# Performance work log

Measured on AMD Instinct MI355X. Metric: run time of the kernel, lower is better.

## Reference

```python
import jax, jax.numpy as jnp
import numpy as np

IMG = 1024.0            # image H = W
PRE_NMS, POST_NMS = 2000, 1000
NMS_THR, MIN_SZ = 0.7, 16.0
B = 16                  # batch of images


def _make_anchors():
    # Standard FPN anchor tiling: strides {4..64}, one scale per level, 3 ratios.
    strides = [4, 8, 16, 32, 64]
    scales = [32.0, 64.0, 128.0, 256.0, 512.0]
    ratios = [0.5, 1.0, 2.0]
    out = []
    for s, sc in zip(strides, scales):
        n = int(IMG) // s
        c = (np.arange(n, dtype=np.float32) + 0.5) * s
        xs, ys = np.meshgrid(c, c, indexing="xy")
        ctr = np.stack([xs.ravel(), ys.ravel()], -1)              # (n*n, 2) cx,cy
        wh = np.array([[sc * np.sqrt(1.0 / r), sc * np.sqrt(r)] for r in ratios],
                      dtype=np.float32)                           # (3, 2)
        b = np.concatenate([ctr[:, None, :] - wh[None] / 2,
                            ctr[:, None, :] + wh[None] / 2], -1)  # (n*n, 3, 4)
        out.append(b.reshape(-1, 4))
    return np.concatenate(out, 0).astype(np.float32)              # (261888, 4)


def setup_inputs() -> dict:
    key = jax.random.key(0)
    k1, k2 = jax.random.split(key)
    anchors = jnp.asarray(_make_anchors())
    A = anchors.shape[0]
    deltas = jax.random.normal(k1, (B, A, 4), dtype=jnp.float32) * 0.1
    scores = jax.random.uniform(k2, (B, A), dtype=jnp.float32)    # post-sigmoid objectness
    return {"anchors": anchors, "deltas": deltas, "scores": scores}


def _decode(anchors, deltas):
    # decode_boxes: deltas (tx,ty,tw,th) applied to anchors; dw/dh clamped at 4.0
    aw = anchors[:, 2] - anchors[:, 0]
    ah = anchors[:, 3] - anchors[:, 1]
    ax = anchors[:, 0] + 0.5 * aw
    ay = anchors[:, 1] + 0.5 * ah
    dx, dy = deltas[..., 0], deltas[..., 1]
    dw = jnp.minimum(deltas[..., 2], 4.0)
    dh = jnp.minimum(deltas[..., 3], 4.0)
    px = dx * aw + ax
    py = dy * ah + ay
    pw = jnp.exp(dw) * aw
    ph = jnp.exp(dh) * ah
    return jnp.stack([px - 0.5 * pw, py - 0.5 * ph,
                      px + 0.5 * pw, py + 0.5 * ph], -1)


def _box_iou(a, b):
    area_a = (a[:, 2] - a[:, 0]) * (a[:, 3] - a[:, 1])
    area_b = (b[:, 2] - b[:, 0]) * (b[:, 3] - b[:, 1])
    lt = jnp.maximum(a[:, None, :2], b[None, :, :2])
    rb = jnp.minimum(a[:, None, 2:], b[None, :, 2:])
    wh = jnp.clip(rb - lt, 0.0)
    inter = wh[..., 0] * wh[..., 1]
    return inter / (area_a[:, None] + area_b[None, :] - inter + 1e-6)


def _filter_one(props, s):
    # RegionProposalNetwork._filter: clip -> size filter -> topk(pre_nms) -> NMS -> post_nms
    x1 = jnp.clip(props[:, 0], 0.0, IMG)
    y1 = jnp.clip(props[:, 1], 0.0, IMG)
    x2 = jnp.clip(props[:, 2], 0.0, IMG)
    y2 = jnp.clip(props[:, 3], 0.0, IMG)
    valid = (x2 - x1 >= MIN_SZ) & (y2 - y1 >= MIN_SZ)
    ms = jnp.where(valid, s, -jnp.inf)                 # mask instead of boolean gather (jit)
    vals, idx = jax.lax.top_k(ms, PRE_NMS)            # sorted desc, as in scores.topk
    b = jnp.stack([x1, y1, x2, y2], -1)[idx]          # (PRE_NMS, 4)
    iou = _box_iou(b, b)                              # (PRE_NMS, PRE_NMS)
    later = jnp.arange(PRE_NMS)

    def body(i, keep):
        # suppress later boxes overlapping a still-kept box i (greedy NMS)
        sup = (iou[i] > NMS_THR) & keep[i] & (later > i)
        return keep & ~sup

    keep = jax.lax.fori_loop(0, PRE_NMS, body, jnp.ones(PRE_NMS, dtype=bool))
    fs = jnp.where(keep, vals, -jnp.inf)
    fv, fi = jax.lax.top_k(fs, POST_NMS)              # kept boxes, desc score order
    good = jnp.isfinite(fv)                           # padding mask for suppressed slots
    boxes = jnp.where(good[:, None], b[fi], 0.0)
    sc = jnp.where(good, fv, 0.0)
    return jnp.concatenate([boxes, sc[:, None]], -1)  # (POST_NMS, 5) = (x1,y1,x2,y2,score)


def reference(anchors, deltas, scores):
    props = _decode(anchors, deltas)                  # (B, A, 4)
    return jax.vmap(_filter_one)(props, scores)       # (B, POST_NMS, 5)
```

## Files before the change

kernel.cpp:

```cpp
#include <hip/hip_runtime.h>
#include <stdint.h>
#include <math.h>


#define IMGF 1024.0f
#define PRE_NMS 2000
#define POST_NMS 1000
#define NMS_THR 0.7f
#define MIN_SZ 16.0f
#define CAP 4096
#define SEL 2048
#define NW (SEL / 64)
#define CNT_STRIDE 32
#define KEY_NEGINF 0x007FFFFFu
#define MAXCHUNK 12
#define IOU_T 0x1.6666668p-1

__device__ __forceinline__ uint32_t f2key(float f) {
  uint32_t u = __float_as_uint(f);
  return (u & 0x80000000u) ? ~u : (u | 0x80000000u);
}
__device__ __forceinline__ float key2f(uint32_t k) {
  uint32_t u = (k & 0x80000000u) ? (k & 0x7FFFFFFFu) : ~k;
  return __uint_as_float(u);
}

__device__ __forceinline__ unsigned long long readlane_u64(unsigned long long v,
                                                           int lane) {
  unsigned int lo = __builtin_amdgcn_readlane((unsigned int)v, lane);
  unsigned int hi = __builtin_amdgcn_readlane((unsigned int)(v >> 32), lane);
  return ((unsigned long long)hi << 32) | lo;
}

__device__ __forceinline__ float4 decode_clip(float4 anc, float4 dlt) {
  float aw = anc.z - anc.x;
  float ah = anc.w - anc.y;
  float ax = anc.x + 0.5f * aw;
  float ay = anc.y + 0.5f * ah;
  float dw = fminf(dlt.z, 4.0f);
  float dh = fminf(dlt.w, 4.0f);
  float px = dlt.x * aw + ax;
  float py = dlt.y * ah + ay;
  float pw = expf(dw) * aw;
  float ph = expf(dh) * ah;
  float x1 = px - 0.5f * pw, y1 = py - 0.5f * ph;
  float x2 = px + 0.5f * pw, y2 = py + 0.5f * ph;
  x1 = fminf(fmaxf(x1, 0.0f), IMGF);
  y1 = fminf(fmaxf(y1, 0.0f), IMGF);
  x2 = fminf(fmaxf(x2, 0.0f), IMGF);
  y2 = fminf(fmaxf(y2, 0.0f), IMGF);
  return make_float4(x1, y1, x2, y2);
}

__global__ void k_decode(const float4* __restrict__ anchors,
                         const float4* __restrict__ deltas,
                         const float* __restrict__ scores,
                         uint32_t* __restrict__ keys,
                         uint32_t* __restrict__ chist,
                         int A, int chunks) {
  int b = blockIdx.y;
  int t = threadIdx.x;
  int lane = t & 63;
  __shared__ uint32_t shist[256];
  shist[t] = 0;
  __syncthreads();
  int base_a = blockIdx.x * (chunks * 256);
  for (int c = 0; c < chunks; c++) {
    int a = base_a + c * 256 + t;
    bool inb = a < A;
    int ac = inb ? a : (A - 1);
    size_t i = (size_t)b * A + ac;
    float4 box = decode_clip(anchors[ac], deltas[i]);
    bool valid = (box.z - box.x >= MIN_SZ) && (box.w - box.y >= MIN_SZ);
    float ms = valid ? scores[i] : -INFINITY;
    uint32_t k = f2key(ms);
    if (inb) keys[i] = k;
    uint32_t bucket = k >> 24;
    bool fin = inb && (k != KEY_NEGINF);
    unsigned long long match = __ballot(fin);
#pragma unroll
    for (int bit = 0; bit < 8; bit++) {
      bool hb = (bucket >> bit) & 1;
      unsigned long long bb = __ballot(hb && fin);
      match &= hb ? bb : ~bb;
    }
    if (fin && (__ffsll((long long)match) - 1 == lane))
      atomicAdd(&shist[bucket], (uint32_t)__popcll(match));
  }
  __syncthreads();
  uint32_t v = shist[t];
  if (v) atomicAdd(&chist[b * 256 + t], v);
}

__global__ void k_coarse(const uint32_t* __restrict__ chist,
                         int* __restrict__ cbArr,
                         uint32_t* __restrict__ cumArr) {
  int b = blockIdx.x;
  int t = threadIdx.x;
  __shared__ uint32_t sA[256];
  sA[t] = chist[b * 256 + t];
  for (int d = 1; d < 256; d <<= 1) {
    __syncthreads();
    uint32_t v = sA[t] + ((t + d < 256) ? sA[t + d] : 0u);
    __syncthreads();
    sA[t] = v;
  }
  __syncthreads();
  if (t == 0 && sA[0] < PRE_NMS) {
    cbArr[b] = -1;
    cumArr[b] = 0;
  }
  uint32_t nxt = (t < 255) ? sA[t + 1] : 0u;
  if (sA[t] >= PRE_NMS && nxt < PRE_NMS) {
    cbArr[b] = t;
    cumArr[b] = nxt;
  }
}

__global__ void k_fine(const uint32_t* __restrict__ keys,
                       const int* __restrict__ cbArr,
                       uint32_t* __restrict__ fhist,
                       int A, int chunks) {
  int b = blockIdx.y;
  int t = threadIdx.x;
  int cb = cbArr[b];
  if (cb < 0) return;
  __shared__ uint32_t shist[256];
  shist[t] = 0;
  __syncthreads();
  int base_a = blockIdx.x * (chunks * 256);
  uint32_t cbu = (uint32_t)cb;
  for (int c = 0; c < chunks; c++) {
    int a = base_a + c * 256 + t;
    if (a >= A) break;
    uint32_t k = keys[(size_t)b * A + a];
    if ((k >> 24) == cbu && k != KEY_NEGINF)
      atomicAdd(&shist[(k >> 16) & 0xFFu], 1u);
  }
  __syncthreads();
  uint32_t v = shist[t];
  if (v) atomicAdd(&fhist[b * 256 + t], v);
}

__global__ void k_thresh(const uint32_t* __restrict__ fhist,
                         const int* __restrict__ cbArr,
                         const uint32_t* __restrict__ cumArr,
                         uint32_t* __restrict__ thresh,
                         uint32_t* __restrict__ cnts) {
  int b = blockIdx.x;
  int t = threadIdx.x;
  __shared__ uint32_t sA[256];
  if (t < 2) cnts[b * CNT_STRIDE + t] = 0;
  int cb = cbArr[b];
  if (cb < 0) {
    if (t == 0) thresh[b] = 0u;
    return;
  }
  uint32_t cumAbove = cumArr[b];
  sA[t] = fhist[b * 256 + t];
  for (int d = 1; d < 256; d <<= 1) {
    __syncthreads();
    uint32_t v = sA[t] + ((t + d < 256) ? sA[t + d] : 0u);
    __syncthreads();
    sA[t] = v;
  }
  __syncthreads();
  uint32_t nxt = (t < 255) ? sA[t + 1] : 0u;
  if (cumAbove + sA[t] >= PRE_NMS && cumAbove + nxt < PRE_NMS)
    thresh[b] = (uint32_t)((cb << 8) | t);
}

__global__ void k_gather(const uint32_t* __restrict__ keys,
                         const uint32_t* __restrict__ thresh,
                         uint32_t* __restrict__ cnts,
                         unsigned long long* __restrict__ cand_sort,
                         float4* __restrict__ sel_box,
                         float* __restrict__ sel_score,
                         int A, int chunks) {
  int b = blockIdx.y;
  int t = threadIdx.x;
  int lane = t & 63;
  int w = t >> 6;
  if (blockIdx.x < SEL / 256) {
    int r = blockIdx.x * 256 + t;
    sel_score[(size_t)b * SEL + r] = -INFINITY;
    sel_box[(size_t)b * SEL + r] = make_float4(0.0f, 0.0f, 0.0f, 0.0f);
  }
  __shared__ unsigned long long s_mA[MAXCHUNK * 4], s_mT[MAXCHUNK * 4];
  __shared__ uint32_t s_offA[MAXCHUNK * 4], s_offT[MAXCHUNK * 4];
  __shared__ uint32_t s_cA[MAXCHUNK * 4], s_cT[MAXCHUNK * 4];
  __shared__ uint32_t s_baseA, s_baseT;
  uint32_t beta = thresh[b];
  uint32_t kreg[MAXCHUNK];
  int base_a = blockIdx.x * (chunks * 256);
  for (int c = 0; c < chunks; c++) {
    int a = base_a + c * 256 + t;
    bool inb = a < A;
    uint32_t k = inb ? keys[(size_t)b * A + a] : KEY_NEGINF;
    kreg[c] = k;
    uint32_t bk = k >> 16;
    bool fin = (k != KEY_NEGINF);
    unsigned long long mA = __ballot(fin && (bk > beta));
    unsigned long long mT = __ballot(fin && (bk == beta));
    if (lane == 0) {
      s_mA[c * 4 + w] = mA;
      s_mT[c * 4 + w] = mT;
    }
  }
  __syncthreads();
  if (t < chunks * 4) {
    s_cA[t] = (uint32_t)__popcll(s_mA[t]);
    s_cT[t] = (uint32_t)__popcll(s_mT[t]);
  }
  __syncthreads();
  if (t == 0) {
    uint32_t accA = 0, accT = 0;
    for (int id = 0; id < chunks * 4; id++) {
      s_offA[id] = accA;
      accA += s_cA[id];
      s_offT[id] = accT;
      accT += s_cT[id];
    }
    s_baseA = accA ? atomicAdd(&cnts[b * CNT_STRIDE + 0], accA) : 0u;
    s_baseT = accT ? atomicAdd(&cnts[b * CNT_STRIDE + 1], accT) : 0u;
  }
  __syncthreads();
  uint32_t baseA = s_baseA, baseT = s_baseT;
  unsigned long long lower = ((unsigned long long)1 << lane) - 1;
  for (int c = 0; c < chunks; c++) {
    int id = c * 4 + w;
    unsigned long long mA = s_mA[id], mT = s_mT[id];
    bool above = (mA >> lane) & 1;
    bool tie = (mT >> lane) & 1;
    if (!(above || tie)) continue;
    int pos;
    if (above) {
      pos = (int)(baseA + s_offA[id] + (uint32_t)__popcll(mA & lower));
      if (pos >= PRE_NMS) continue;
    } else {
      pos = CAP - 1 - (int)(baseT + s_offT[id] + (uint32_t)__popcll(mT & lower));
      if (pos < PRE_NMS) continue;
    }
    int a = base_a + c * 256 + t;
    cand_sort[(size_t)b * CAP + pos] =
        ((unsigned long long)kreg[c] << 32) | (uint32_t)(~(uint32_t)a);
  }
}

__global__ void k_rank(const unsigned long long* __restrict__ cand_sort,
                       const uint32_t* __restrict__ cnts,
                       const float4* __restrict__ anchors,
                       const float4* __restrict__ deltas,
                       float4* __restrict__ sel_box,
                       float* __restrict__ sel_score, int A) {
  int b = blockIdx.y;
  int t = threadIdx.x;
  uint32_t c1 = cnts[b * CNT_STRIDE + 0];
  if (c1 > PRE_NMS) c1 = PRE_NMS;
  uint32_t c2 = cnts[b * CNT_STRIDE + 1];
  if (c2 > CAP - PRE_NMS) c2 = CAP - PRE_NMS;
  int loTie = CAP - (int)c2;
  int bs = blockIdx.x * 256;
  if (bs >= (int)c1 && bs + 256 <= loTie) return;
  int s = bs + t;
  bool live = (s < (int)c1) || (s >= loTie);
  unsigned long long myKey = live ? cand_sort[(size_t)b * CAP + s] : 0ull;
  __shared__ unsigned long long tile[256];
  int rank = 0;
  for (int ts = 0; ts < CAP; ts += 256) {
    if (ts >= (int)c1 && ts + 256 <= loTie) continue;
    int idx = ts + t;
    bool lv = (idx < (int)c1) || (idx >= loTie);
    __syncthreads();
    tile[t] = lv ? cand_sort[(size_t)b * CAP + idx] : 0ull;
    __syncthreads();
    if (live) {
#pragma unroll 8
      for (int j = 0; j < 256; j++) rank += (tile[j] > myKey) ? 1 : 0;
    }
  }
  if (live && rank < SEL) {
    uint32_t a = ~((uint32_t)myKey);
    float4 box = decode_clip(anchors[a], deltas[(size_t)b * A + a]);
    sel_score[(size_t)b * SEL + rank] = key2f((uint32_t)(myKey >> 32));
    sel_box[(size_t)b * SEL + rank] = box;
  }
}

__global__ void __launch_bounds__(256)
k_nmsmask(const float4* __restrict__ sel_box,
          unsigned long long* __restrict__ mask,
          unsigned long long* __restrict__ maskT) {
  int qb = blockIdx.x;
  int ib = blockIdx.y;
  if (qb * 4 + 3 < ib) return;
  int b = blockIdx.z;
  int t = threadIdx.x;
  int lane = t & 63;
  int w = t >> 6;
  int jb = qb * 4 + w;
  __shared__ float4 rowb[64];
  __shared__ float rowarea[64];
  __shared__ float4 colb[4][64];
  __shared__ float colarea[4][64];
  if (t < 64) {
    float4 rb = sel_box[(size_t)b * SEL + ib * 64 + t];
    rowb[t] = rb;
    rowarea[t] = (rb.z - rb.x) * (rb.w - rb.y);
  }
  bool wvalid = (jb >= ib);
  if (wvalid) {
    float4 cbx = sel_box[(size_t)b * SEL + jb * 64 + lane];
    colb[w][lane] = cbx;
    colarea[w][lane] = (cbx.z - cbx.x) * (cbx.w - cbx.y);
  }
  __syncthreads();
  if (!wvalid) return;
  float4 a = rowb[lane];
  float area_a = rowarea[lane];
  int i = ib * 64 + lane;
  unsigned long long bits = 0ull;
  if (i < PRE_NMS) {
    bool diag = (jb == ib);
    int jmax = min(64, PRE_NMS - jb * 64);
    for (int jj = 0; jj < jmax; jj++) {
      if (diag && jj <= lane) continue;
      float4 bb = colb[w][jj];
      float area_b = colarea[w][jj];
      float ltx = fmaxf(a.x, bb.x), lty = fmaxf(a.y, bb.y);
      float rbx = fminf(a.z, bb.z), rby = fminf(a.w, bb.w);
      float ww = fmaxf(rbx - ltx, 0.0f), hh = fmaxf(rby - lty, 0.0f);
      float inter = ww * hh;
      float denom = area_a + area_b - inter + 1e-6f;
      if ((double)inter >= IOU_T * (double)denom) bits |= (1ull << jj);
    }
  }
  mask[((size_t)b * NW + jb) * SEL + i] = bits;
  if (jb == ib) {
    unsigned long long myT = 0ull;
#pragma unroll 1
    for (int jj = 0; jj < 64; jj++) {
      unsigned long long colw = __ballot((bits >> jj) & 1ull);
      if (lane == jj) myT = colw;
    }
    maskT[(size_t)b * SEL + i] = myT;
  }
}

__global__ void __launch_bounds__(64, 1)
k_scanout(const float4* __restrict__ sel_box,
          const float* __restrict__ sel_score,
          const unsigned long long* __restrict__ mask,
          const unsigned long long* __restrict__ maskT,
          float* __restrict__ out) {
  int b = blockIdx.x;
  int t = threadIdx.x;
  int tw = t & 31;
  __shared__ uint32_t keptList[POST_NMS + 64];
  __shared__ unsigned long long tile[2][64 * NW];
  unsigned long long removed = 0ull;
  int kc = 0;
  const unsigned long long* mb = mask + (size_t)b * NW * SEL;
  const unsigned long long* tbase = maskT + (size_t)b * SEL;
  const int lastChunk = (PRE_NMS - 1) / 64;
  int cjb = t >> 5;
  int ro = (t & 31) * 2;

  {
#pragma unroll
    for (int k = 0; k < 16; k++) {
      const unsigned long long* gp =
          mb + ((size_t)(2 * k + cjb)) * SEL + ro;
      __builtin_amdgcn_global_load_lds(
          (const __attribute__((address_space(1))) uint32_t*)gp,
          (__attribute__((address_space(3))) uint32_t*)&tile[0][k * 128],
          16, 0, 0);
    }
  }
  unsigned long long colm = tbase[t];
  uint32_t scb = __float_as_uint(sel_score[(size_t)b * SEL + t]);

  for (int chunk = 0; chunk <= lastChunk; chunk++) {
    int cur = chunk & 1;
    unsigned long long colm_n = 0ull;
    uint32_t scb_n = 0xFF800000u;
    if (chunk < lastChunk) {
#pragma unroll
      for (int k = 0; k < 16; k++) {
        const unsigned long long* gp =
            mb + ((size_t)(2 * k + cjb)) * SEL + (size_t)(chunk + 1) * 64 + ro;
        __builtin_amdgcn_global_load_lds(
            (const __attribute__((address_space(1))) uint32_t*)gp,
            (__attribute__((address_space(3))) uint32_t*)
                &tile[cur ^ 1][k * 128],
            16, 0, 0);
      }
      colm_n = tbase[(chunk + 1) * 64 + t];
      scb_n =
          __float_as_uint(sel_score[(size_t)b * SEL + (chunk + 1) * 64 + t]);
    }
    int rmax = PRE_NMS - chunk * 64;
    if (rmax > 64) rmax = 64;
    unsigned long long vb = __ballot(scb != 0xFF800000u);
    unsigned long long curw = readlane_u64(removed, chunk);
    unsigned long long range = (rmax >= 64) ? ~0ull : ((1ull << rmax) - 1ull);
    unsigned long long alive0 = ~curw & range;
    unsigned long long K = alive0;
    bool aliveb = (alive0 >> t) & 1ull;
#pragma unroll 1
    for (int it = 0; it < 64; ++it) {
      bool deadb = (colm & K) != 0ull;
      unsigned long long Kn = __ballot(aliveb && !deadb);
      if (Kn == K) break;
      K = Kn;
    }
    unsigned long long keptbits = K;
    unsigned long long kv = keptbits & vb;
    if ((kv >> t) & 1ull) {
      int rank = (int)__popcll(kv & ((1ull << t) - 1ull));
      keptList[kc + rank] = (uint32_t)(chunk * 64 + t);
    }
    kc += (int)__popcll(kv);
    if (kc >= POST_NMS) break;
    if (chunk == lastChunk) break;
    asm volatile("s_waitcnt vmcnt(18)" ::: "memory");
    __builtin_amdgcn_sched_barrier(0);
    unsigned long long acc = 0ull;
#pragma unroll
    for (int j = 0; j < 64; j++) {
      int jr = (j + tw) & 63;
      unsigned long long v = tile[cur][tw * 64 + jr];
      unsigned long long mk =
          (unsigned long long)(-(long long)((keptbits >> jr) & 1ull));
      acc |= v & mk;
    }
    unsigned long long wv = (tw >= chunk) ? ~0ull : 0ull;
    removed |= acc & wv;
    __builtin_amdgcn_sched_barrier(0);
    colm = colm_n;
    scb = scb_n;
  }
  int kcc = kc < POST_NMS ? kc : POST_NMS;
  __syncthreads();
  for (int r = t; r < POST_NMS; r += 64) {
    float4 bx = make_float4(0.0f, 0.0f, 0.0f, 0.0f);
    float sc = 0.0f;
    if (r < kcc) {
      int i = (int)keptList[r];
      bx = sel_box[(size_t)b * SEL + i];
      sc = sel_score[(size_t)b * SEL + i];
    }
    float* o = out + ((size_t)b * POST_NMS + r) * 5;
    o[0] = bx.x;
    o[1] = bx.y;
    o[2] = bx.z;
    o[3] = bx.w;
    o[4] = sc;
  }
}

extern "C" void kernel_launch(void* const* d_in, const int* in_sizes, int n_in,
                              void* d_out, int out_size, void* d_ws, size_t ws_size,
                              hipStream_t stream) {
  const float* anchors = (const float*)d_in[0];
  const float* deltas = (const float*)d_in[1];
  const float* scores = (const float*)d_in[2];
  int A = in_sizes[0] / 4;
  int BA = in_sizes[2];
  int B = BA / A;
  float* out = (float*)d_out;

  char* ws = (char*)d_ws;
  size_t off = 0;
  uint32_t* keys = (uint32_t*)(ws + off);
  off += (size_t)BA * 4;
  uint32_t* chist = (uint32_t*)(ws + off);
  off += (size_t)B * 256 * 4;
  uint32_t* fhist = (uint32_t*)(ws + off);
  off += (size_t)B * 256 * 4;
  int* cbArr = (int*)(ws + off);
  off += (size_t)B * 4;
  uint32_t* cumArr = (uint32_t*)(ws + off);
  off += (size_t)B * 4;
  uint32_t* thresh = (uint32_t*)(ws + off);
  off += (size_t)B * 4;
  off = (off + 127) & ~(size_t)127;
  uint32_t* cnts = (uint32_t*)(ws + off);
  off += (size_t)B * CNT_STRIDE * 4;
  off = (off + 15) & ~(size_t)15;
  unsigned long long* cand_sort = (unsigned long long*)(ws + off);
  off += (size_t)B * CAP * 8;
  float4* sel_box = (float4*)(ws + off);
  off += (size_t)B * SEL * 16;
  float* sel_score = (float*)(ws + off);
  off += (size_t)B * SEL * 4;
  unsigned long long* mask = (unsigned long long*)(ws + off);
  off += (size_t)B * NW * SEL * 8;
  unsigned long long* maskT = (unsigned long long*)(ws + off);
  off += (size_t)B * SEL * 8;

  int chunks = (A % (256 * 11) == 0) ? 11 : 1;
  int bpb = (A + 256 * chunks - 1) / (256 * chunks);

  hipMemsetAsync(chist, 0, (size_t)B * 256 * 4 * 2, stream);
  k_decode<<<dim3(bpb, B), 256, 0, stream>>>((const float4*)anchors,
                                             (const float4*)deltas, scores,
                                             keys, chist, A, chunks);
  k_coarse<<<B, 256, 0, stream>>>(chist, cbArr, cumArr);
  k_fine<<<dim3(bpb, B), 256, 0, stream>>>(keys, cbArr, fhist, A, chunks);
  k_thresh<<<B, 256, 0, stream>>>(fhist, cbArr, cumArr, thresh, cnts);
  k_gather<<<dim3(bpb, B), 256, 0, stream>>>(keys, thresh, cnts, cand_sort,
                                             sel_box, sel_score, A, chunks);
  k_rank<<<dim3(CAP / 256, B), 256, 0, stream>>>(cand_sort, cnts,
                                                 (const float4*)anchors,
                                                 (const float4*)deltas,
                                                 sel_box, sel_score, A);
  k_nmsmask<<<dim3(8, NW, B), 256, 0, stream>>>(sel_box, mask, maskT);
  k_scanout<<<B, 64, 0, stream>>>(sel_box, sel_score, mask, maskT, out);
}
```

Measured before the change: 279.3 us.

## Split rank computation into parallel tile-pair count kernel plus scatter kernel

The rank-by-counting kernel previously looped each block over all key tiles serially. It is now split into k_rankcnt, which gives every (self tile, key tile) pair its own block and writes partial counts, and k_scatter, which sums the partials and decodes and scatters the selected boxes. This exposes up to 16x more blocks and uses 128-bit shared loads, to fix low occupancy in the rank step. In exchange it adds a kernel launch and a global round trip for the partial counts, stored by reusing the keys buffer.

```diff
diff --git a/kernel.cpp b/kernel.cpp
--- a/kernel.cpp
+++ b/kernel.cpp
@@ -247,39 +247,68 @@
   }
 }
 
-__global__ void k_rank(const unsigned long long* __restrict__ cand_sort,
-                       const uint32_t* __restrict__ cnts,
-                       const float4* __restrict__ anchors,
-                       const float4* __restrict__ deltas,
-                       float4* __restrict__ sel_box,
-                       float* __restrict__ sel_score, int A) {
-  int b = blockIdx.y;
+__global__ void k_rankcnt(const unsigned long long* __restrict__ cand_sort,
+                          const uint32_t* __restrict__ cnts,
+                          uint32_t* __restrict__ rnk_partial) {
+  int st = blockIdx.x;
+  int kt = blockIdx.y;
+  int b = blockIdx.z;
   int t = threadIdx.x;
   uint32_t c1 = cnts[b * CNT_STRIDE + 0];
   if (c1 > PRE_NMS) c1 = PRE_NMS;
   uint32_t c2 = cnts[b * CNT_STRIDE + 1];
   if (c2 > CAP - PRE_NMS) c2 = CAP - PRE_NMS;
   int loTie = CAP - (int)c2;
-  int bs = blockIdx.x * 256;
+  int bs = st * 256, ks = kt * 256;
+  if (bs >= (int)c1 && bs + 256 <= loTie) return;
+  if (ks >= (int)c1 && ks + 256 <= loTie) return;
+  int s = bs + t;
+  bool live = (s < (int)c1) || (s >= loTie);
+  unsigned long long myKey = live ? cand_sort[(size_t)b * CAP + s] : 0ull;
+  __shared__ __attribute__((aligned(16))) unsigned long long tile[256];
+  int idx = ks + t;
+  bool lv = (idx < (int)c1) || (idx >= loTie);
+  tile[t] = lv ? cand_sort[(size_t)b * CAP + idx] : 0ull;
+  __syncthreads();
+  const ulonglong2* tile2 = (const ulonglong2*)tile;
+  int cnt = 0;
+#pragma unroll 8
+  for (int j = 0; j < 128; j++) {
+    ulonglong2 v = tile2[j];
+    cnt += (v.x > myKey) ? 1 : 0;
+    cnt += (v.y > myKey) ? 1 : 0;
+  }
+  rnk_partial[((size_t)b * 16 + kt) * CAP + s] = (uint32_t)cnt;
+}
+
+__global__ void k_scatter(const unsigned long long* __restrict__ cand_sort,
+                          const uint32_t* __restrict__ rnk_partial,
+                          const uint32_t* __restrict__ cnts,
+                          const float4* __restrict__ anchors,
+                          const float4* __restrict__ deltas,
+                          float4* __restrict__ sel_box,
+                          float* __restrict__ sel_score, int A) {
+  int st = blockIdx.x;
+  int b = blockIdx.y;
+  int t = threadIdx.x;
+  uint32_t c1 = cnts[b * CNT_STRIDE + 0];
+  if (c1 > PRE_NMS) c1 = PRE_NMS;
+  uint32_t c2 = cnts[b * CNT_STRIDE + 1];
+  if (c2 > CAP - PRE_NMS) c2 = CAP - PRE_NMS;
+  int loTie = CAP - (int)c2;
+  int bs = st * 256;
   if (bs >= (int)c1 && bs + 256 <= loTie) return;
   int s = bs + t;
   bool live = (s < (int)c1) || (s >= loTie);
-  unsigned long long myKey = live ? cand_sort[(size_t)b * CAP + s] : 0ull;
-  __shared__ unsigned long long tile[256];
+  if (!live) return;
   int rank = 0;
-  for (int ts = 0; ts < CAP; ts += 256) {
-    if (ts >= (int)c1 && ts + 256 <= loTie) continue;
-    int idx = ts + t;
-    bool lv = (idx < (int)c1) || (idx >= loTie);
-    __syncthreads();
-    tile[t] = lv ? cand_sort[(size_t)b * CAP + idx] : 0ull;
-    __syncthreads();
-    if (live) {
-#pragma unroll 8
-      for (int j = 0; j < 256; j++) rank += (tile[j] > myKey) ? 1 : 0;
-    }
-  }
-  if (live && rank < SEL) {
+  for (int kt = 0; kt < 16; kt++) {
+    int ks = kt * 256;
+    if (ks >= (int)c1 && ks + 256 <= loTie) continue;
+    rank += (int)rnk_partial[((size_t)b * 16 + kt) * CAP + s];
+  }
+  if (rank < SEL) {
+    unsigned long long myKey = cand_sort[(size_t)b * CAP + s];
     uint32_t a = ~((uint32_t)myKey);
     float4 box = decode_clip(anchors[a], deltas[(size_t)b * A + a]);
     sel_score[(size_t)b * SEL + rank] = key2f((uint32_t)(myKey >> 32));
@@ -498,6 +527,7 @@
   off += (size_t)B * NW * SEL * 8;
   unsigned long long* maskT = (unsigned long long*)(ws + off);
   off += (size_t)B * SEL * 8;
+  uint32_t* rnk_partial = keys;
 
   int chunks = (A % (256 * 11) == 0) ? 11 : 1;
   int bpb = (A + 256 * chunks - 1) / (256 * chunks);
@@ -511,10 +541,12 @@
   k_thresh<<<B, 256, 0, stream>>>(fhist, cbArr, cumArr, thresh, cnts);
   k_gather<<<dim3(bpb, B), 256, 0, stream>>>(keys, thresh, cnts, cand_sort,
                                              sel_box, sel_score, A, chunks);
-  k_rank<<<dim3(CAP / 256, B), 256, 0, stream>>>(cand_sort, cnts,
-                                                 (const float4*)anchors,
-                                                 (const float4*)deltas,
-                                                 sel_box, sel_score, A);
+  k_rankcnt<<<dim3(CAP / 256, CAP / 256, B), 256, 0, stream>>>(cand_sort, cnts,
+                                                               rnk_partial);
+  k_scatter<<<dim3(CAP / 256, B), 256, 0, stream>>>(cand_sort, rnk_partial,
+                                                    cnts, (const float4*)anchors,
+                                                    (const float4*)deltas,
+                                                    sel_box, sel_score, A);
   k_nmsmask<<<dim3(8, NW, B), 256, 0, stream>>>(sel_box, mask, maskT);
   k_scanout<<<B, 64, 0, stream>>>(sel_box, sel_score, mask, maskT, out);
 }
```

Result: faster. 247.3 us (-11.5%).
